# Kernel tuning notes

Hardware: AMD Instinct MI355X
Metric: run time of the kernel (lower is better)

## Reference

```python
import jax, jax.numpy as jnp
import numpy as np

N = 16384       # num nodes
E = 65536       # num edges (before self loops)
IN_DIM = 1536
HID = 1024
HEADS = 8
HD = HID // HEADS  # 128
NEG_SLOPE = 0.2
EPS = 1e-5


def _xavier(key, shape):
    fan_in, fan_out = shape[0], shape[-1]
    s = jnp.sqrt(6.0 / (fan_in + fan_out)).astype(jnp.float32)
    return jax.random.uniform(key, shape, jnp.float32, -s, s)


def setup_inputs() -> dict:
    key = jax.random.key(0)
    ks = jax.random.split(key, 32)
    inp = {
        "x": jax.random.normal(ks[0], (N, IN_DIM), jnp.float32),
        "edge_index": jax.random.randint(ks[1], (2, E), 0, N, dtype=jnp.int32),
        # input projection + norm1
        "W_in": _xavier(ks[2], (IN_DIM, HID)), "b_in": jnp.zeros((HID,), jnp.float32),
        "ln1_g": jnp.ones((HID,), jnp.float32), "ln1_b": jnp.zeros((HID,), jnp.float32),
        # GATv2 layer 1
        "g1_Wl": _xavier(ks[3], (HID, HID)), "g1_bl": jnp.zeros((HID,), jnp.float32),
        "g1_Wr": _xavier(ks[4], (HID, HID)), "g1_br": jnp.zeros((HID,), jnp.float32),
        "g1_att": _xavier(ks[5], (HEADS, HD)), "g1_bo": jnp.zeros((HID,), jnp.float32),
        "ln2_g": jnp.ones((HID,), jnp.float32), "ln2_b": jnp.zeros((HID,), jnp.float32),
        # GATv2 layer 2
        "g2_Wl": _xavier(ks[6], (HID, HID)), "g2_bl": jnp.zeros((HID,), jnp.float32),
        "g2_Wr": _xavier(ks[7], (HID, HID)), "g2_br": jnp.zeros((HID,), jnp.float32),
        "g2_att": _xavier(ks[8], (HEADS, HD)), "g2_bo": jnp.zeros((HID,), jnp.float32),
        "ln3_g": jnp.ones((HID,), jnp.float32), "ln3_b": jnp.zeros((HID,), jnp.float32),
        # scorer MLP 1024 -> 512 -> 128 -> 1
        "Ws1": _xavier(ks[9], (HID, 512)), "bs1": jnp.zeros((512,), jnp.float32),
        "Ws2": _xavier(ks[10], (512, 128)), "bs2": jnp.zeros((128,), jnp.float32),
        "Ws3": _xavier(ks[11], (128, 1)), "bs3": jnp.zeros((1,), jnp.float32),
    }
    return inp


def layer_norm(x, g, b):
    mu = jnp.mean(x, axis=-1, keepdims=True)
    var = jnp.var(x, axis=-1, keepdims=True)
    return (x - mu) * jax.lax.rsqrt(var + EPS) * g + b


def gatv2(h, src, dst, Wl, bl, Wr, br, att, bo):
    # GATv2Conv: x_j = lin_l(h)[src], x_i = lin_r(h)[dst]
    xl = (h @ Wl + bl).reshape(N, HEADS, HD)
    xr = (h @ Wr + br).reshape(N, HEADS, HD)
    e = jax.nn.leaky_relu(xl[src] + xr[dst], NEG_SLOPE)      # [E', H, C]
    logit = jnp.einsum('ehc,hc->eh', e, att)                  # [E', H]
    m = jax.ops.segment_max(logit, dst, num_segments=N)       # segment softmax over dst
    a = jnp.exp(logit - m[dst])
    denom = jax.ops.segment_sum(a, dst, num_segments=N)
    alpha = a / denom[dst]
    out = jax.ops.segment_sum(alpha[:, :, None] * xl[src], dst, num_segments=N)
    return out.reshape(N, HID) + bo


def reference(x, edge_index, W_in, b_in, ln1_g, ln1_b,
              g1_Wl, g1_bl, g1_Wr, g1_br, g1_att, g1_bo, ln2_g, ln2_b,
              g2_Wl, g2_bl, g2_Wr, g2_br, g2_att, g2_bo, ln3_g, ln3_b,
              Ws1, bs1, Ws2, bs2, Ws3, bs3):
    # PyG GATv2Conv adds self-loops by default
    loop = jnp.arange(N, dtype=edge_index.dtype)
    src = jnp.concatenate([edge_index[0], loop])
    dst = jnp.concatenate([edge_index[1], loop])

    h = jax.nn.gelu(layer_norm(x @ W_in + b_in, ln1_g, ln1_b), approximate=False)
    h1 = gatv2(h, src, dst, g1_Wl, g1_bl, g1_Wr, g1_br, g1_att, g1_bo)
    h = h + jax.nn.gelu(layer_norm(h1, ln2_g, ln2_b), approximate=False)
    h2 = gatv2(h, src, dst, g2_Wl, g2_bl, g2_Wr, g2_br, g2_att, g2_bo)
    h = h + jax.nn.gelu(layer_norm(h2, ln3_g, ln3_b), approximate=False)

    s = jax.nn.silu(h @ Ws1 + bs1)
    s = jax.nn.silu(s @ Ws2 + bs2)
    scores = (s @ Ws3 + bs3).squeeze(-1)   # [N]
    return scores, h
```

## Files before the change

kernel.cpp:

```cpp
#include <hip/hip_runtime.h>
#include <hip/hip_bf16.h>
#include <math.h>

#define N_NODES 16384
#define E_EDGES 65536
#define ET (E_EDGES + N_NODES)
#define IN_DIM 1536
#define HID 1024
#define XSTR 2048

typedef __attribute__((ext_vector_type(8))) short bf16x8;
typedef __attribute__((ext_vector_type(4))) float f32x4;

__device__ __forceinline__ unsigned short f2b(float f) {
  unsigned int u = __float_as_uint(f);
  u = (u + 0x7FFFu + ((u >> 16) & 1u)) >> 16;
  return (unsigned short)u;
}

__device__ __forceinline__ float b2f(unsigned short u) {
  return __uint_as_float((unsigned int)u << 16);
}

__device__ __forceinline__ void gload_lds16(const void* g, void* l) {
  __builtin_amdgcn_global_load_lds((const __attribute__((address_space(1))) void*)g,
                                   (__attribute__((address_space(3))) void*)l, 16, 0, 0);
}

__device__ __forceinline__ float gelu_exact(float y) {
  return 0.5f * y * (1.0f + erff(y * 0.70710678118654752f));
}

__global__ void conv_bf16_kernel(const float* __restrict__ in, unsigned short* __restrict__ out, int n4) {
  int i = blockIdx.x * 256 + threadIdx.x;
  if (i < n4) {
    float4 v = ((const float4*)in)[i];
    ushort4 o;
    o.x = f2b(v.x); o.y = f2b(v.y); o.z = f2b(v.z); o.w = f2b(v.w);
    ((ushort4*)out)[i] = o;
  }
}

__global__ void transpose_all_kernel(const float* __restrict__ W_in,
                                     const float* __restrict__ g1Wl, const float* __restrict__ g1Wr,
                                     const float* __restrict__ g2Wl, const float* __restrict__ g2Wr,
                                     const float* __restrict__ Ws1, const float* __restrict__ Ws2,
                                     unsigned short* __restrict__ WinT, unsigned short* __restrict__ g1WT,
                                     unsigned short* __restrict__ g2WT, unsigned short* __restrict__ Ws1T,
                                     unsigned short* __restrict__ Ws2T) {
  int bid = blockIdx.x;
  const float* src; unsigned short* dst; int K, N, tile;
  if (bid < 1536)      { src = W_in; dst = WinT;                          K = 1536; N = 1024; tile = bid; }
  else if (bid < 2560) { src = g1Wl; dst = g1WT;                         K = 1024; N = 1024; tile = bid - 1536; }
  else if (bid < 3584) { src = g1Wr; dst = g1WT + (size_t)1024 * 1024;   K = 1024; N = 1024; tile = bid - 2560; }
  else if (bid < 4608) { src = g2Wl; dst = g2WT;                         K = 1024; N = 1024; tile = bid - 3584; }
  else if (bid < 5632) { src = g2Wr; dst = g2WT + (size_t)1024 * 1024;   K = 1024; N = 1024; tile = bid - 4608; }
  else if (bid < 6144) { src = Ws1; dst = Ws1T;                          K = 1024; N = 512;  tile = bid - 5632; }
  else                 { src = Ws2; dst = Ws2T;                          K = 512;  N = 128;  tile = bid - 6144; }
  int nxt = N >> 5;
  int bx = (tile % nxt) * 32;
  int by = (tile / nxt) * 32;
  __shared__ float tilebuf[32][33];
  int tx = threadIdx.x, ty = threadIdx.y;
  #pragma unroll
  for (int i = 0; i < 32; i += 8)
    tilebuf[ty + i][tx] = src[(size_t)(by + ty + i) * N + bx + tx];
  __syncthreads();
  #pragma unroll
  for (int i = 0; i < 32; i += 8)
    dst[(size_t)(bx + ty + i) * K + by + tx] = f2b(tilebuf[tx][ty + i]);
}

template <int ACT, int WB>
__global__ __launch_bounds__(512)
void gemm_bf16_kernel(const unsigned short* __restrict__ A, const unsigned short* __restrict__ Bt,
                      const float* __restrict__ bias, const float* __restrict__ bias2, int nsplit,
                      float* __restrict__ C, unsigned short* __restrict__ Cb,
                      int M, int N, int K, int nx) {
  __shared__ unsigned short As[256 * 64];
  __shared__ unsigned short Bs[128 * 64];
  const int t = threadIdx.x;
  const int l = t & 63;
  const int w = t >> 6;
  const int wr = w >> 1, wc = w & 1;

  const int nwg = gridDim.x;
  const int bid = blockIdx.x;
  int tile = bid;
  if ((nwg & 7) == 0) {
    const int cpx = nwg >> 3;
    tile = (bid & 7) * cpx + (bid >> 3);
  }
  const int bm = (tile / nx) * 256;
  const int bn = (tile % nx) * 128;

  f32x4 acc[4][4];
  #pragma unroll
  for (int m = 0; m < 4; m++)
    #pragma unroll
    for (int n = 0; n < 4; n++) acc[m][n] = (f32x4){0.f, 0.f, 0.f, 0.f};

  const int srow = t >> 3;
  const int scolbsw = ((t & 7) * 16) ^ ((srow & 7) << 4);
  const unsigned short* Ag = A + (size_t)(bm + srow) * K + (scolbsw >> 1);
  const unsigned short* Bg = Bt + (size_t)(bn + srow) * K + (scolbsw >> 1);

  const int ar = wr * 64 + (l & 15);
  const int br = wc * 64 + (l & 15);
  const int kk2 = (l >> 4) * 16;
  const int swA = (ar & 7) << 4;
  const int swB = (br & 7) << 4;
  const char* Asb = (const char*)As;
  const char* Bsb = (const char*)Bs;

  for (int k0 = 0; k0 < K; k0 += 64) {
    #pragma unroll
    for (int i = 0; i < 4; i++)
      gload_lds16(Ag + (size_t)i * 64 * K + k0, (char*)As + t * 16 + i * 8192);
    #pragma unroll
    for (int i = 0; i < 2; i++)
      gload_lds16(Bg + (size_t)i * 64 * K + k0, (char*)Bs + t * 16 + i * 8192);
    __syncthreads();
    bf16x8 af[4], bfr[4];
    #pragma unroll
    for (int kh = 0; kh < 2; kh++) {
      const int kb = kk2 + kh * 64;
      #pragma unroll
      for (int m = 0; m < 4; m++)
        af[m] = *(const bf16x8*)(Asb + (ar + m * 16) * 128 + (kb ^ swA));
      #pragma unroll
      for (int n = 0; n < 4; n++)
        bfr[n] = *(const bf16x8*)(Bsb + (br + n * 16) * 128 + (kb ^ swB));
      #pragma unroll
      for (int m = 0; m < 4; m++)
        #pragma unroll
        for (int n = 0; n < 4; n++)
          acc[m][n] = __builtin_amdgcn_mfma_f32_16x16x32_bf16(af[m], bfr[n], acc[m][n], 0, 0, 0);
    }
    __syncthreads();
  }

  const int crow0 = bm + wr * 64 + (l >> 4) * 4;
  const int ccol0 = bn + wc * 64 + (l & 15);
  #pragma unroll
  for (int m = 0; m < 4; m++) {
    #pragma unroll
    for (int n = 0; n < 4; n++) {
      int col = ccol0 + n * 16;
      float bv = (col < nsplit) ? bias[col] : bias2[col - nsplit];
      #pragma unroll
      for (int v = 0; v < 4; v++) {
        int row = crow0 + m * 16 + v;
        float x = acc[m][n][v] + bv;
        if (ACT == 1) x = x / (1.0f + expf(-x));
        if (WB != 2) C[(size_t)row * N + col] = x;
        if (WB != 0) Cb[(size_t)row * N + col] = f2b(x);
      }
    }
  }
}

__global__ __launch_bounds__(256)
void ln_gelu_kernel(const unsigned short* __restrict__ cb, const float* __restrict__ g,
                    const float* __restrict__ b, unsigned short* __restrict__ hb) {
  int row = blockIdx.x;
  int t = threadIdx.x;
  int c0 = t * 4;
  ushort4 u = *(const ushort4*)(cb + (size_t)row * HID + c0);
  float v0 = b2f(u.x), v1 = b2f(u.y), v2 = b2f(u.z), v3 = b2f(u.w);
  float s = v0 + v1 + v2 + v3;
  float q = v0 * v0 + v1 * v1 + v2 * v2 + v3 * v3;
  #pragma unroll
  for (int off = 32; off; off >>= 1) {
    s += __shfl_xor(s, off);
    q += __shfl_xor(q, off);
  }
  __shared__ float rs[4], rq[4];
  int wv = t >> 6, l = t & 63;
  if (l == 0) { rs[wv] = s; rq[wv] = q; }
  __syncthreads();
  s = rs[0] + rs[1] + rs[2] + rs[3];
  q = rq[0] + rq[1] + rq[2] + rq[3];
  float mu = s * (1.0f / HID);
  float var = q * (1.0f / HID) - mu * mu;
  float rstd = rsqrtf(var + 1e-5f);
  const float4 gv = *(const float4*)(g + c0);
  const float4 bv = *(const float4*)(b + c0);
  ushort4 ob;
  ob.x = f2b(gelu_exact((v0 - mu) * rstd * gv.x + bv.x));
  ob.y = f2b(gelu_exact((v1 - mu) * rstd * gv.y + bv.y));
  ob.z = f2b(gelu_exact((v2 - mu) * rstd * gv.z + bv.z));
  ob.w = f2b(gelu_exact((v3 - mu) * rstd * gv.w + bv.w));
  *(ushort4*)(hb + (size_t)row * HID + c0) = ob;
}

__global__ void build_edges_kernel(const int* __restrict__ ei, int* __restrict__ srcA,
                                   int* __restrict__ dstA, int* __restrict__ deg) {
  int i = blockIdx.x * 256 + threadIdx.x;
  if (i >= ET) return;
  int s, d;
  if (i < E_EDGES) { s = ei[i]; d = ei[E_EDGES + i]; }
  else             { s = i - E_EDGES; d = s; }
  srcA[i] = s;
  dstA[i] = d;
  atomicAdd(&deg[d], 1);
}

__global__ __launch_bounds__(1024)
void scan16k_kernel(const int* __restrict__ deg, int* __restrict__ rowstart) {
  __shared__ int s[1024];
  int t = threadIdx.x;
  int local[16];
  int sum = 0;
  #pragma unroll
  for (int i = 0; i < 16; i++) { local[i] = deg[t * 16 + i]; sum += local[i]; }
  s[t] = sum;
  __syncthreads();
  for (int off = 1; off < 1024; off <<= 1) {
    int v = (t >= off) ? s[t - off] : 0;
    __syncthreads();
    s[t] += v;
    __syncthreads();
  }
  int run = s[t] - sum;
  #pragma unroll
  for (int i = 0; i < 16; i++) { rowstart[t * 16 + i] = run; run += local[i]; }
  if (t == 1023) rowstart[16384] = run;
}

__global__ void scatter_edges_kernel(const int* __restrict__ srcA, const int* __restrict__ dstA,
                                     const int* __restrict__ rowstart, int* __restrict__ cursor,
                                     int* __restrict__ src_csr) {
  int i = blockIdx.x * 256 + threadIdx.x;
  if (i >= ET) return;
  int d = dstA[i];
  int pos = atomicAdd(&cursor[d], 1);
  src_csr[rowstart[d] + pos] = srcA[i];
}

template <int WRITE_H>
__global__ __launch_bounds__(256)
void gat_fused_kernel(const unsigned short* __restrict__ xe, const float* __restrict__ att,
                      const int* __restrict__ src_csr, const int* __restrict__ rowstart,
                      const float* __restrict__ bo, const float* __restrict__ lng,
                      const float* __restrict__ lnb, float* __restrict__ h,
                      unsigned short* __restrict__ hb) {
  const int l = threadIdx.x & 63;
  const int nid = blockIdx.x * 4 + (threadIdx.x >> 6);
  const int beg = rowstart[nid], end = rowstart[nid + 1];
  const int cb = l * 16;

  float xrf[16], attf[16];
  {
    const unsigned short* xrd = xe + (size_t)nid * XSTR + 1024 + cb;
    bf16x8 r0 = *(const bf16x8*)xrd;
    bf16x8 r1 = *(const bf16x8*)(xrd + 8);
    #pragma unroll
    for (int j = 0; j < 8; j++) {
      xrf[j] = b2f((unsigned short)r0[j]);
      xrf[j + 8] = b2f((unsigned short)r1[j]);
    }
    #pragma unroll
    for (int j = 0; j < 4; j++) {
      float4 a = *(const float4*)(att + cb + j * 4);
      attf[j * 4] = a.x; attf[j * 4 + 1] = a.y;
      attf[j * 4 + 2] = a.z; attf[j * 4 + 3] = a.w;
    }
  }

  float m = -1e30f, den = 0.f;
  float acc[16];
  #pragma unroll
  for (int j = 0; j < 16; j++) acc[j] = 0.f;

  bf16x8 xa0, xa1, xb0, xb1;
  if (beg < end) {
    const unsigned short* p = xe + (size_t)src_csr[beg] * XSTR + cb;
    xa0 = *(const bf16x8*)p;
    xa1 = *(const bf16x8*)(p + 8);
  }
  if (beg + 1 < end) {
    const unsigned short* p = xe + (size_t)src_csr[beg + 1] * XSTR + cb;
    xb0 = *(const bf16x8*)p;
    xb1 = *(const bf16x8*)(p + 8);
  }
  for (int e = beg; e < end; ++e) {
    bf16x8 c0 = xa0, c1 = xa1;
    xa0 = xb0; xa1 = xb1;
    if (e + 2 < end) {
      const unsigned short* p = xe + (size_t)src_csr[e + 2] * XSTR + cb;
      xb0 = *(const bf16x8*)p;
      xb1 = *(const bf16x8*)(p + 8);
    }
    float xf[16];
    #pragma unroll
    for (int j = 0; j < 8; j++) {
      xf[j] = b2f((unsigned short)c0[j]);
      xf[j + 8] = b2f((unsigned short)c1[j]);
    }
    float lg = 0.f;
    #pragma unroll
    for (int j = 0; j < 16; j++) {
      float u = xf[j] + xrf[j];
      u = fmaxf(u, 0.2f * u);
      lg = fmaf(u, attf[j], lg);
    }
    lg += __shfl_xor(lg, 1);
    lg += __shfl_xor(lg, 2);
    lg += __shfl_xor(lg, 4);
    if (__all(lg <= m + 8.f)) {
      float wgt = expf(lg - m);
      den += wgt;
      #pragma unroll
      for (int j = 0; j < 16; j++) acc[j] = fmaf(wgt, xf[j], acc[j]);
    } else {
      float nm = fmaxf(m, lg);
      float sc = expf(m - nm);
      float wgt = expf(lg - nm);
      den = den * sc + wgt;
      #pragma unroll
      for (int j = 0; j < 16; j++) acc[j] = fmaf(wgt, xf[j], acc[j] * sc);
      m = nm;
    }
  }

  float inv = 1.0f / den;
  float v[16];
  #pragma unroll
  for (int j = 0; j < 4; j++) {
    float4 b = *(const float4*)(bo + cb + j * 4);
    v[j * 4] = acc[j * 4] * inv + b.x;
    v[j * 4 + 1] = acc[j * 4 + 1] * inv + b.y;
    v[j * 4 + 2] = acc[j * 4 + 2] * inv + b.z;
    v[j * 4 + 3] = acc[j * 4 + 3] * inv + b.w;
  }
  float s = 0.f, q = 0.f;
  #pragma unroll
  for (int j = 0; j < 16; j++) { s += v[j]; q += v[j] * v[j]; }
  #pragma unroll
  for (int off = 32; off; off >>= 1) {
    s += __shfl_xor(s, off);
    q += __shfl_xor(q, off);
  }
  float mu = s * (1.0f / HID);
  float var = q * (1.0f / HID) - mu * mu;
  float rstd = rsqrtf(var + 1e-5f);

  float* hr = h + (size_t)nid * HID + cb;
  unsigned short* hbr = hb + (size_t)nid * HID + cb;
  #pragma unroll
  for (int j = 0; j < 4; j++) {
    float4 gv = *(const float4*)(lng + cb + j * 4);
    float4 bb = *(const float4*)(lnb + cb + j * 4);
    ushort4 hu = *(const ushort4*)(hbr + j * 4);
    float o0 = b2f(hu.x) + gelu_exact((v[j * 4] - mu) * rstd * gv.x + bb.x);
    float o1 = b2f(hu.y) + gelu_exact((v[j * 4 + 1] - mu) * rstd * gv.y + bb.y);
    float o2 = b2f(hu.z) + gelu_exact((v[j * 4 + 2] - mu) * rstd * gv.z + bb.z);
    float o3 = b2f(hu.w) + gelu_exact((v[j * 4 + 3] - mu) * rstd * gv.w + bb.w);
    if (WRITE_H) *(float4*)(hr + j * 4) = (float4){o0, o1, o2, o3};
    ushort4 ob;
    ob.x = f2b(o0); ob.y = f2b(o1); ob.z = f2b(o2); ob.w = f2b(o3);
    *(ushort4*)(hbr + j * 4) = ob;
  }
}

__global__ __launch_bounds__(256)
void score_kernel(const float* __restrict__ s2, const float* __restrict__ Ws3,
                  const float* __restrict__ bs3, float* __restrict__ out) {
  int nid = blockIdx.x * 4 + (threadIdx.x >> 6);
  int l = threadIdx.x & 63;
  const float* r = s2 + (size_t)nid * 128;
  float a = r[l] * Ws3[l] + r[l + 64] * Ws3[l + 64];
  #pragma unroll
  for (int off = 32; off; off >>= 1) a += __shfl_xor(a, off);
  if (l == 0) out[nid] = a + bs3[0];
}

extern "C" void kernel_launch(void* const* d_in, const int* in_sizes, int n_in,
                              void* d_out, int out_size, void* d_ws, size_t ws_size,
                              hipStream_t stream) {
  const float* x    = (const float*)d_in[0];
  const int*   ei   = (const int*)  d_in[1];
  const float* W_in = (const float*)d_in[2];
  const float* b_in = (const float*)d_in[3];
  const float* ln1g = (const float*)d_in[4];
  const float* ln1b = (const float*)d_in[5];
  const float* g1Wl = (const float*)d_in[6];
  const float* g1bl = (const float*)d_in[7];
  const float* g1Wr = (const float*)d_in[8];
  const float* g1br = (const float*)d_in[9];
  const float* g1att= (const float*)d_in[10];
  const float* g1bo = (const float*)d_in[11];
  const float* ln2g = (const float*)d_in[12];
  const float* ln2b = (const float*)d_in[13];
  const float* g2Wl = (const float*)d_in[14];
  const float* g2bl = (const float*)d_in[15];
  const float* g2Wr = (const float*)d_in[16];
  const float* g2br = (const float*)d_in[17];
  const float* g2att= (const float*)d_in[18];
  const float* g2bo = (const float*)d_in[19];
  const float* ln3g = (const float*)d_in[20];
  const float* ln3b = (const float*)d_in[21];
  const float* Ws1  = (const float*)d_in[22];
  const float* bs1  = (const float*)d_in[23];
  const float* Ws2  = (const float*)d_in[24];
  const float* bs2  = (const float*)d_in[25];
  const float* Ws3  = (const float*)d_in[26];
  const float* bs3  = (const float*)d_in[27];

  float* scores = (float*)d_out;
  float* h      = (float*)d_out + N_NODES;

  char* wsp = (char*)d_ws;
  size_t off = 0;
  auto alloc = [&](size_t bytes) -> char* {
    char* p = wsp + off;
    off += (bytes + 255) & ~(size_t)255;
    return p;
  };
  unsigned short* xb    = (unsigned short*)alloc((size_t)N_NODES * IN_DIM * 2);
  unsigned short* WinT  = (unsigned short*)alloc((size_t)HID * IN_DIM * 2);
  unsigned short* g1WT  = (unsigned short*)alloc((size_t)XSTR * HID * 2);
  unsigned short* g2WT  = (unsigned short*)alloc((size_t)XSTR * HID * 2);
  unsigned short* Ws1T  = (unsigned short*)alloc((size_t)512 * HID * 2);
  unsigned short* Ws2T  = (unsigned short*)alloc((size_t)128 * 512 * 2);
  unsigned short* hb    = (unsigned short*)alloc((size_t)N_NODES * HID * 2);
  unsigned short* s1b   = (unsigned short*)alloc((size_t)N_NODES * 512 * 2);
  unsigned short* xe    = (unsigned short*)alloc((size_t)N_NODES * XSTR * 2);
  float* C      = (float*)alloc((size_t)N_NODES * HID * 4);
  int* srcA     = (int*)alloc((size_t)ET * 4);
  int* dstA     = (int*)alloc((size_t)ET * 4);
  int* deg      = (int*)alloc(65536);
  int* cursor   = (int*)alloc(65536);
  int* rowstart = (int*)alloc(65544);
  int* src_csr  = (int*)alloc((size_t)ET * 4);
  unsigned short* cbp = (unsigned short*)C;

  conv_bf16_kernel<<<(N_NODES * IN_DIM / 4 + 255) / 256, 256, 0, stream>>>(x, xb, N_NODES * IN_DIM / 4);
  transpose_all_kernel<<<6208, dim3(32, 8), 0, stream>>>(W_in, g1Wl, g1Wr, g2Wl, g2Wr, Ws1, Ws2,
                                                         WinT, g1WT, g2WT, Ws1T, Ws2T);

  hipMemsetAsync(deg, 0, 131072, stream);
  build_edges_kernel<<<ET / 256, 256, 0, stream>>>(ei, srcA, dstA, deg);
  scan16k_kernel<<<1, 1024, 0, stream>>>(deg, rowstart);
  scatter_edges_kernel<<<ET / 256, 256, 0, stream>>>(srcA, dstA, rowstart, cursor, src_csr);

  gemm_bf16_kernel<0, 2><<<(N_NODES / 256) * (HID / 128), 512, 0, stream>>>(
      xb, WinT, b_in, b_in, HID, nullptr, cbp, N_NODES, HID, IN_DIM, HID / 128);
  ln_gelu_kernel<<<N_NODES, 256, 0, stream>>>(cbp, ln1g, ln1b, hb);

  gemm_bf16_kernel<0, 2><<<(N_NODES / 256) * (XSTR / 128), 512, 0, stream>>>(
      hb, g1WT, g1bl, g1br, HID, nullptr, xe, N_NODES, XSTR, HID, XSTR / 128);
  gat_fused_kernel<0><<<N_NODES / 4, 256, 0, stream>>>(xe, g1att, src_csr, rowstart, g1bo,
                                                       ln2g, ln2b, h, hb);

  gemm_bf16_kernel<0, 2><<<(N_NODES / 256) * (XSTR / 128), 512, 0, stream>>>(
      hb, g2WT, g2bl, g2br, HID, nullptr, xe, N_NODES, XSTR, HID, XSTR / 128);
  gat_fused_kernel<1><<<N_NODES / 4, 256, 0, stream>>>(xe, g2att, src_csr, rowstart, g2bo,
                                                       ln3g, ln3b, h, hb);

  gemm_bf16_kernel<1, 2><<<(N_NODES / 256) * (512 / 128), 512, 0, stream>>>(
      hb, Ws1T, bs1, bs1, 512, nullptr, s1b, N_NODES, 512, HID, 512 / 128);
  gemm_bf16_kernel<1, 0><<<(N_NODES / 256) * 1, 512, 0, stream>>>(
      s1b, Ws2T, bs2, bs2, 128, C, nullptr, N_NODES, 128, 512, 1);
  score_kernel<<<N_NODES / 4, 256, 0, stream>>>(C, Ws3, bs3, scores);
}
```

Baseline: 440.3 us.

## Fuse fp32-to-bf16 input conversion into first GEMM; grid-stride GAT kernel

```diff
diff --git a/kernel.cpp b/kernel.cpp
--- a/kernel.cpp
+++ b/kernel.cpp
@@ -29,16 +29,6 @@
 
 __device__ __forceinline__ float gelu_exact(float y) {
   return 0.5f * y * (1.0f + erff(y * 0.70710678118654752f));
-}
-
-__global__ void conv_bf16_kernel(const float* __restrict__ in, unsigned short* __restrict__ out, int n4) {
-  int i = blockIdx.x * 256 + threadIdx.x;
-  if (i < n4) {
-    float4 v = ((const float4*)in)[i];
-    ushort4 o;
-    o.x = f2b(v.x); o.y = f2b(v.y); o.z = f2b(v.z); o.w = f2b(v.w);
-    ((ushort4*)out)[i] = o;
-  }
 }
 
 __global__ void transpose_all_kernel(const float* __restrict__ W_in,
@@ -71,9 +61,9 @@
     dst[(size_t)(bx + ty + i) * K + by + tx] = f2b(tilebuf[tx][ty + i]);
 }
 
-template <int ACT, int WB>
+template <int ACT, int WB, int FP32A>
 __global__ __launch_bounds__(512)
-void gemm_bf16_kernel(const unsigned short* __restrict__ A, const unsigned short* __restrict__ Bt,
+void gemm_bf16_kernel(const void* __restrict__ Av, const unsigned short* __restrict__ Bt,
                       const float* __restrict__ bias, const float* __restrict__ bias2, int nsplit,
                       float* __restrict__ C, unsigned short* __restrict__ Cb,
                       int M, int N, int K, int nx) {
@@ -102,7 +92,8 @@
 
   const int srow = t >> 3;
   const int scolbsw = ((t & 7) * 16) ^ ((srow & 7) << 4);
-  const unsigned short* Ag = A + (size_t)(bm + srow) * K + (scolbsw >> 1);
+  const unsigned short* Ag = (const unsigned short*)Av + (size_t)(bm + srow) * K + (scolbsw >> 1);
+  const float* Ag32 = (const float*)Av + (size_t)(bm + srow) * K + (scolbsw >> 1);
   const unsigned short* Bg = Bt + (size_t)(bn + srow) * K + (scolbsw >> 1);
 
   const int ar = wr * 64 + (l & 15);
@@ -114,9 +105,24 @@
   const char* Bsb = (const char*)Bs;
 
   for (int k0 = 0; k0 < K; k0 += 64) {
-    #pragma unroll
-    for (int i = 0; i < 4; i++)
-      gload_lds16(Ag + (size_t)i * 64 * K + k0, (char*)As + t * 16 + i * 8192);
+    if (FP32A) {
+      #pragma unroll
+      for (int i = 0; i < 4; i++) {
+        const float* s = Ag32 + (size_t)i * 64 * K + k0;
+        float4 f0 = *(const float4*)s;
+        float4 f1 = *(const float4*)(s + 4);
+        bf16x8 wv;
+        wv[0] = (short)f2b(f0.x); wv[1] = (short)f2b(f0.y);
+        wv[2] = (short)f2b(f0.z); wv[3] = (short)f2b(f0.w);
+        wv[4] = (short)f2b(f1.x); wv[5] = (short)f2b(f1.y);
+        wv[6] = (short)f2b(f1.z); wv[7] = (short)f2b(f1.w);
+        *(bf16x8*)((char*)As + t * 16 + i * 8192) = wv;
+      }
+    } else {
+      #pragma unroll
+      for (int i = 0; i < 4; i++)
+        gload_lds16(Ag + (size_t)i * 64 * K + k0, (char*)As + t * 16 + i * 8192);
+    }
     #pragma unroll
     for (int i = 0; i < 2; i++)
       gload_lds16(Bg + (size_t)i * 64 * K + k0, (char*)Bs + t * 16 + i * 8192);
@@ -246,121 +252,126 @@
                       const float* __restrict__ lnb, float* __restrict__ h,
                       unsigned short* __restrict__ hb) {
   const int l = threadIdx.x & 63;
-  const int nid = blockIdx.x * 4 + (threadIdx.x >> 6);
-  const int beg = rowstart[nid], end = rowstart[nid + 1];
   const int cb = l * 16;
-
-  float xrf[16], attf[16];
-  {
-    const unsigned short* xrd = xe + (size_t)nid * XSTR + 1024 + cb;
-    bf16x8 r0 = *(const bf16x8*)xrd;
-    bf16x8 r1 = *(const bf16x8*)(xrd + 8);
-    #pragma unroll
-    for (int j = 0; j < 8; j++) {
-      xrf[j] = b2f((unsigned short)r0[j]);
-      xrf[j + 8] = b2f((unsigned short)r1[j]);
-    }
-    #pragma unroll
-    for (int j = 0; j < 4; j++) {
-      float4 a = *(const float4*)(att + cb + j * 4);
-      attf[j * 4] = a.x; attf[j * 4 + 1] = a.y;
-      attf[j * 4 + 2] = a.z; attf[j * 4 + 3] = a.w;
-    }
-  }
-
-  float m = -1e30f, den = 0.f;
-  float acc[16];
-  #pragma unroll
-  for (int j = 0; j < 16; j++) acc[j] = 0.f;
-
-  bf16x8 xa0, xa1, xb0, xb1;
-  if (beg < end) {
-    const unsigned short* p = xe + (size_t)src_csr[beg] * XSTR + cb;
-    xa0 = *(const bf16x8*)p;
-    xa1 = *(const bf16x8*)(p + 8);
-  }
-  if (beg + 1 < end) {
-    const unsigned short* p = xe + (size_t)src_csr[beg + 1] * XSTR + cb;
-    xb0 = *(const bf16x8*)p;
-    xb1 = *(const bf16x8*)(p + 8);
-  }
-  for (int e = beg; e < end; ++e) {
-    bf16x8 c0 = xa0, c1 = xa1;
-    xa0 = xb0; xa1 = xb1;
-    if (e + 2 < end) {
-      const unsigned short* p = xe + (size_t)src_csr[e + 2] * XSTR + cb;
+  const int stride = gridDim.x * 4;
+
+  float attf[16];
+  #pragma unroll
+  for (int j = 0; j < 4; j++) {
+    float4 a = *(const float4*)(att + cb + j * 4);
+    attf[j * 4] = a.x; attf[j * 4 + 1] = a.y;
+    attf[j * 4 + 2] = a.z; attf[j * 4 + 3] = a.w;
+  }
+
+  for (int nid = blockIdx.x * 4 + (threadIdx.x >> 6); nid < N_NODES; nid += stride) {
+    const int beg = rowstart[nid], end = rowstart[nid + 1];
+
+    float xrf[16];
+    {
+      const unsigned short* xrd = xe + (size_t)nid * XSTR + 1024 + cb;
+      bf16x8 r0 = *(const bf16x8*)xrd;
+      bf16x8 r1 = *(const bf16x8*)(xrd + 8);
+      #pragma unroll
+      for (int j = 0; j < 8; j++) {
+        xrf[j] = b2f((unsigned short)r0[j]);
+        xrf[j + 8] = b2f((unsigned short)r1[j]);
+      }
+    }
+
+    float m = -1e30f, den = 0.f;
+    float acc[16];
+    #pragma unroll
+    for (int j = 0; j < 16; j++) acc[j] = 0.f;
+
+    bf16x8 xa0, xa1, xb0, xb1;
+    if (beg < end) {
+      const unsigned short* p = xe + (size_t)src_csr[beg] * XSTR + cb;
+      xa0 = *(const bf16x8*)p;
+      xa1 = *(const bf16x8*)(p + 8);
+    }
+    if (beg + 1 < end) {
+      const unsigned short* p = xe + (size_t)src_csr[beg + 1] * XSTR + cb;
       xb0 = *(const bf16x8*)p;
       xb1 = *(const bf16x8*)(p + 8);
     }
-    float xf[16];
-    #pragma unroll
-    for (int j = 0; j < 8; j++) {
-      xf[j] = b2f((unsigned short)c0[j]);
-      xf[j + 8] = b2f((unsigned short)c1[j]);
-    }
-    float lg = 0.f;
-    #pragma unroll
-    for (int j = 0; j < 16; j++) {
-      float u = xf[j] + xrf[j];
-      u = fmaxf(u, 0.2f * u);
-      lg = fmaf(u, attf[j], lg);
-    }
-    lg += __shfl_xor(lg, 1);
-    lg += __shfl_xor(lg, 2);
-    lg += __shfl_xor(lg, 4);
-    if (__all(lg <= m + 8.f)) {
-      float wgt = expf(lg - m);
-      den += wgt;
-      #pragma unroll
-      for (int j = 0; j < 16; j++) acc[j] = fmaf(wgt, xf[j], acc[j]);
-    } else {
-      float nm = fmaxf(m, lg);
-      float sc = expf(m - nm);
-      float wgt = expf(lg - nm);
-      den = den * sc + wgt;
-      #pragma unroll
-      for (int j = 0; j < 16; j++) acc[j] = fmaf(wgt, xf[j], acc[j] * sc);
-      m = nm;
-    }
-  }
-
-  float inv = 1.0f / den;
-  float v[16];
-  #pragma unroll
-  for (int j = 0; j < 4; j++) {
-    float4 b = *(const float4*)(bo + cb + j * 4);
-    v[j * 4] = acc[j * 4] * inv + b.x;
-    v[j * 4 + 1] = acc[j * 4 + 1] * inv + b.y;
-    v[j * 4 + 2] = acc[j * 4 + 2] * inv + b.z;
-    v[j * 4 + 3] = acc[j * 4 + 3] * inv + b.w;
-  }
-  float s = 0.f, q = 0.f;
-  #pragma unroll
-  for (int j = 0; j < 16; j++) { s += v[j]; q += v[j] * v[j]; }
-  #pragma unroll
-  for (int off = 32; off; off >>= 1) {
-    s += __shfl_xor(s, off);
-    q += __shfl_xor(q, off);
-  }
-  float mu = s * (1.0f / HID);
-  float var = q * (1.0f / HID) - mu * mu;
-  float rstd = rsqrtf(var + 1e-5f);
-
-  float* hr = h + (size_t)nid * HID + cb;
-  unsigned short* hbr = hb + (size_t)nid * HID + cb;
-  #pragma unroll
-  for (int j = 0; j < 4; j++) {
-    float4 gv = *(const float4*)(lng + cb + j * 4);
-    float4 bb = *(const float4*)(lnb + cb + j * 4);
-    ushort4 hu = *(const ushort4*)(hbr + j * 4);
-    float o0 = b2f(hu.x) + gelu_exact((v[j * 4] - mu) * rstd * gv.x + bb.x);
-    float o1 = b2f(hu.y) + gelu_exact((v[j * 4 + 1] - mu) * rstd * gv.y + bb.y);
-    float o2 = b2f(hu.z) + gelu_exact((v[j * 4 + 2] - mu) * rstd * gv.z + bb.z);
-    float o3 = b2f(hu.w) + gelu_exact((v[j * 4 + 3] - mu) * rstd * gv.w + bb.w);
-    if (WRITE_H) *(float4*)(hr + j * 4) = (float4){o0, o1, o2, o3};
-    ushort4 ob;
-    ob.x = f2b(o0); ob.y = f2b(o1); ob.z = f2b(o2); ob.w = f2b(o3);
-    *(ushort4*)(hbr + j * 4) = ob;
+    for (int e = beg; e < end; ++e) {
+      bf16x8 c0 = xa0, c1 = xa1;
+      xa0 = xb0; xa1 = xb1;
+      if (e + 2 < end) {
+        const unsigned short* p = xe + (size_t)src_csr[e + 2] * XSTR + cb;
+        xb0 = *(const bf16x8*)p;
+        xb1 = *(const bf16x8*)(p + 8);
+      }
+      float xf[16];
+      #pragma unroll
+      for (int j = 0; j < 8; j++) {
+        xf[j] = b2f((unsigned short)c0[j]);
+        xf[j + 8] = b2f((unsigned short)c1[j]);
+      }
+      float lg = 0.f;
+      #pragma unroll
+      for (int j = 0; j < 16; j++) {
+        float u = xf[j] + xrf[j];
+        u = fmaxf(u, 0.2f * u);
+        lg = fmaf(u, attf[j], lg);
+      }
+      lg += __shfl_xor(lg, 1);
+      lg += __shfl_xor(lg, 2);
+      lg += __shfl_xor(lg, 4);
+      if (__all(lg <= m + 8.f)) {
+        float wgt = expf(lg - m);
+        den += wgt;
+        #pragma unroll
+        for (int j = 0; j < 16; j++) acc[j] = fmaf(wgt, xf[j], acc[j]);
+      } else {
+        float nm = fmaxf(m, lg);
+        float sc = expf(m - nm);
+        float wgt = expf(lg - nm);
+        den = den * sc + wgt;
+        #pragma unroll
+        for (int j = 0; j < 16; j++) acc[j] = fmaf(wgt, xf[j], acc[j] * sc);
+        m = nm;
+      }
+    }
+
+    float inv = 1.0f / den;
+    float v[16];
+    #pragma unroll
+    for (int j = 0; j < 4; j++) {
+      float4 b = *(const float4*)(bo + cb + j * 4);
+      v[j * 4] = acc[j * 4] * inv + b.x;
+      v[j * 4 + 1] = acc[j * 4 + 1] * inv + b.y;
+      v[j * 4 + 2] = acc[j * 4 + 2] * inv + b.z;
+      v[j * 4 + 3] = acc[j * 4 + 3] * inv + b.w;
+    }
+    float s = 0.f, q = 0.f;
+    #pragma unroll
+    for (int j = 0; j < 16; j++) { s += v[j]; q += v[j] * v[j]; }
+    #pragma unroll
+    for (int off = 32; off; off >>= 1) {
+      s += __shfl_xor(s, off);
+      q += __shfl_xor(q, off);
+    }
+    float mu = s * (1.0f / HID);
+    float var = q * (1.0f / HID) - mu * mu;
+    float rstd = rsqrtf(var + 1e-5f);
+
+    float* hr = h + (size_t)nid * HID + cb;
+    unsigned short* hbr = hb + (size_t)nid * HID + cb;
+    #pragma unroll
+    for (int j = 0; j < 4; j++) {
+      float4 gv = *(const float4*)(lng + cb + j * 4);
+      float4 bb = *(const float4*)(lnb + cb + j * 4);
+      ushort4 hu = *(const ushort4*)(hbr + j * 4);
+      float o0 = b2f(hu.x) + gelu_exact((v[j * 4] - mu) * rstd * gv.x + bb.x);
+      float o1 = b2f(hu.y) + gelu_exact((v[j * 4 + 1] - mu) * rstd * gv.y + bb.y);
+      float o2 = b2f(hu.z) + gelu_exact((v[j * 4 + 2] - mu) * rstd * gv.z + bb.z);
+      float o3 = b2f(hu.w) + gelu_exact((v[j * 4 + 3] - mu) * rstd * gv.w + bb.w);
+      if (WRITE_H) *(float4*)(hr + j * 4) = (float4){o0, o1, o2, o3};
+      ushort4 ob;
+      ob.x = f2b(o0); ob.y = f2b(o1); ob.z = f2b(o2); ob.w = f2b(o3);
+      *(ushort4*)(hbr + j * 4) = ob;
+    }
   }
 }
 
@@ -418,7 +429,6 @@
     off += (bytes + 255) & ~(size_t)255;
     return p;
   };
-  unsigned short* xb    = (unsigned short*)alloc((size_t)N_NODES * IN_DIM * 2);
   unsigned short* WinT  = (unsigned short*)alloc((size_t)HID * IN_DIM * 2);
   unsigned short* g1WT  = (unsigned short*)alloc((size_t)XSTR * HID * 2);
   unsigned short* g2WT  = (unsigned short*)alloc((size_t)XSTR * HID * 2);
@@ -436,7 +446,6 @@
   int* src_csr  = (int*)alloc((size_t)ET * 4);
   unsigned short* cbp = (unsigned short*)C;
 
-  conv_bf16_kernel<<<(N_NODES * IN_DIM / 4 + 255) / 256, 256, 0, stream>>>(x, xb, N_NODES * IN_DIM / 4);
   transpose_all_kernel<<<6208, dim3(32, 8), 0, stream>>>(W_in, g1Wl, g1Wr, g2Wl, g2Wr, Ws1, Ws2,
                                                          WinT, g1WT, g2WT, Ws1T, Ws2T);
 
@@ -445,23 +454,23 @@
   scan16k_kernel<<<1, 1024, 0, stream>>>(deg, rowstart);
   scatter_edges_kernel<<<ET / 256, 256, 0, stream>>>(srcA, dstA, rowstart, cursor, src_csr);
 
-  gemm_bf16_kernel<0, 2><<<(N_NODES / 256) * (HID / 128), 512, 0, stream>>>(
-      xb, WinT, b_in, b_in, HID, nullptr, cbp, N_NODES, HID, IN_DIM, HID / 128);
+  gemm_bf16_kernel<0, 2, 1><<<(N_NODES / 256) * (HID / 128), 512, 0, stream>>>(
+      x, WinT, b_in, b_in, HID, nullptr, cbp, N_NODES, HID, IN_DIM, HID / 128);
   ln_gelu_kernel<<<N_NODES, 256, 0, stream>>>(cbp, ln1g, ln1b, hb);
 
-  gemm_bf16_kernel<0, 2><<<(N_NODES / 256) * (XSTR / 128), 512, 0, stream>>>(
+  gemm_bf16_kernel<0, 2, 0><<<(N_NODES / 256) * (XSTR / 128), 512, 0, stream>>>(
       hb, g1WT, g1bl, g1br, HID, nullptr, xe, N_NODES, XSTR, HID, XSTR / 128);
-  gat_fused_kernel<0><<<N_NODES / 4, 256, 0, stream>>>(xe, g1att, src_csr, rowstart, g1bo,
-                                                       ln2g, ln2b, h, hb);
-
-  gemm_bf16_kernel<0, 2><<<(N_NODES / 256) * (XSTR / 128), 512, 0, stream>>>(
+  gat_fused_kernel<0><<<2048, 256, 0, stream>>>(xe, g1att, src_csr, rowstart, g1bo,
+                                                ln2g, ln2b, h, hb);
+
+  gemm_bf16_kernel<0, 2, 0><<<(N_NODES / 256) * (XSTR / 128), 512, 0, stream>>>(
       hb, g2WT, g2bl, g2br, HID, nullptr, xe, N_NODES, XSTR, HID, XSTR / 128);
-  gat_fused_kernel<1><<<N_NODES / 4, 256, 0, stream>>>(xe, g2att, src_csr, rowstart, g2bo,
-                                                       ln3g, ln3b, h, hb);
-
-  gemm_bf16_kernel<1, 2><<<(N_NODES / 256) * (512 / 128), 512, 0, stream>>>(
+  gat_fused_kernel<1><<<2048, 256, 0, stream>>>(xe, g2att, src_csr, rowstart, g2bo,
+                                                ln3g, ln3b, h, hb);
+
+  gemm_bf16_kernel<1, 2, 0><<<(N_NODES / 256) * (512 / 128), 512, 0, stream>>>(
       hb, Ws1T, bs1, bs1, 512, nullptr, s1b, N_NODES, 512, HID, 512 / 128);
-  gemm_bf16_kernel<1, 0><<<(N_NODES / 256) * 1, 512, 0, stream>>>(
+  gemm_bf16_kernel<1, 0, 0><<<(N_NODES / 256) * 1, 512, 0, stream>>>(
       s1b, Ws2T, bs2, bs2, 128, C, nullptr, N_NODES, 128, 512, 1);
   score_kernel<<<N_NODES / 4, 256, 0, stream>>>(C, Ws3, bs3, scores);
 }
```

New measurement: 482.0 us. +9.5%, slower.

## Add 256x256-tile 8-wave GEMM with phased LDS double-buffered pipeline

Applied to the files above, without the earlier changes.

```diff
diff --git a/kernel.cpp b/kernel.cpp
--- a/kernel.cpp
+++ b/kernel.cpp
@@ -69,6 +69,137 @@
   #pragma unroll
   for (int i = 0; i < 32; i += 8)
     dst[(size_t)(bx + ty + i) * K + by + tx] = f2b(tilebuf[tx][ty + i]);
+}
+
+#define VM4() asm volatile("s_waitcnt vmcnt(4)" ::: "memory")
+#define VM0() asm volatile("s_waitcnt vmcnt(0)" ::: "memory")
+
+#define STGA(kh, Tn)                                                           \
+  do {                                                                         \
+    const unsigned short* s_ = Ag + (size_t)(Tn) * 64 + (kh) * 32;             \
+    gload_lds16(s_, Anxt + (kh) * 16384 + t * 16);                             \
+    gload_lds16(s_ + rowK128, Anxt + (kh) * 16384 + 8192 + t * 16);            \
+  } while (0)
+#define STGB(kh, Tn)                                                           \
+  do {                                                                         \
+    const unsigned short* s_ = Bg + (size_t)(Tn) * 64 + (kh) * 32;             \
+    gload_lds16(s_, Bnxt + (kh) * 16384 + t * 16);                             \
+    gload_lds16(s_ + rowK128, Bnxt + (kh) * 16384 + 8192 + t * 16);            \
+  } while (0)
+
+#define PHASE(kh, mh, STG_STMT, VM_STMT)                                       \
+  {                                                                            \
+    const char* Ap_ = Acur + (kh) * 16384;                                     \
+    const char* Bp_ = Bcur + (kh) * 16384;                                     \
+    bf16x8 af_[4], bf_[4];                                                     \
+    _Pragma("unroll") for (int m_ = 0; m_ < 4; m_++)                           \
+      af_[m_] = *(const bf16x8*)(Ap_ + (ar + ((mh) * 4 + m_) * 16) * 64 + (kk2 ^ swA)); \
+    _Pragma("unroll") for (int n_ = 0; n_ < 4; n_++)                           \
+      bf_[n_] = *(const bf16x8*)(Bp_ + (br + n_ * 16) * 64 + (kk2 ^ swB));     \
+    STG_STMT;                                                                  \
+    VM_STMT;                                                                   \
+    asm volatile("" ::: "memory");                                             \
+    __builtin_amdgcn_s_barrier();                                              \
+    asm volatile("s_waitcnt lgkmcnt(0)" ::: "memory");                         \
+    __builtin_amdgcn_sched_barrier(0);                                         \
+    __builtin_amdgcn_s_setprio(1);                                             \
+    _Pragma("unroll") for (int m_ = 0; m_ < 4; m_++)                           \
+      _Pragma("unroll") for (int n_ = 0; n_ < 4; n_++)                         \
+        acc[(mh) * 4 + m_][n_] = __builtin_amdgcn_mfma_f32_16x16x32_bf16(      \
+            af_[m_], bf_[n_], acc[(mh) * 4 + m_][n_], 0, 0, 0);                \
+    __builtin_amdgcn_s_setprio(0);                                             \
+    asm volatile("" ::: "memory");                                             \
+    __builtin_amdgcn_s_barrier();                                              \
+  }
+
+template <int WB>
+__global__ __launch_bounds__(512, 1)
+void gemm8p_kernel(const unsigned short* __restrict__ A, const unsigned short* __restrict__ Bt,
+                   const float* __restrict__ bias, const float* __restrict__ bias2, int nsplit,
+                   float* __restrict__ C, unsigned short* __restrict__ Cb,
+                   int M, int N, int K, int nx) {
+  __shared__ char Abuf[2][32768];
+  __shared__ char Bbuf[2][32768];
+  const int t = threadIdx.x;
+  const int l = t & 63;
+  const int w = t >> 6;
+  const int wr = w >> 2, wc = w & 3;
+
+  const int nwg = gridDim.x;
+  const int cpx = nwg >> 3;
+  const int bid = blockIdx.x;
+  const int tl = (bid & 7) * cpx + (bid >> 3);
+  const int bm = (tl / nx) * 256;
+  const int bn = (tl % nx) * 256;
+
+  f32x4 acc[8][4];
+  #pragma unroll
+  for (int m = 0; m < 8; m++)
+    #pragma unroll
+    for (int n = 0; n < 4; n++) acc[m][n] = (f32x4){0.f, 0.f, 0.f, 0.f};
+
+  const int srow = t >> 2;
+  const int scolb = ((t & 3) * 16) ^ (((srow >> 1) & 3) << 4);
+  const unsigned short* Ag = A + (size_t)(bm + srow) * K + (scolb >> 1);
+  const unsigned short* Bg = Bt + (size_t)(bn + srow) * K + (scolb >> 1);
+  const size_t rowK128 = (size_t)128 * K;
+
+  const int ar = wr * 128 + (l & 15);
+  const int br = wc * 64 + (l & 15);
+  const int kk2 = (l >> 4) * 16;
+  const int swA = ((ar >> 1) & 3) << 4;
+  const int swB = ((br >> 1) & 3) << 4;
+
+  const int NT = K >> 6;
+
+  gload_lds16(Ag, Abuf[0] + t * 16);
+  gload_lds16(Ag + rowK128, Abuf[0] + 8192 + t * 16);
+  gload_lds16(Bg, Bbuf[0] + t * 16);
+  gload_lds16(Bg + rowK128, Bbuf[0] + 8192 + t * 16);
+  gload_lds16(Ag + 32, Abuf[0] + 16384 + t * 16);
+  gload_lds16(Ag + 32 + rowK128, Abuf[0] + 16384 + 8192 + t * 16);
+  gload_lds16(Bg + 32, Bbuf[0] + 16384 + t * 16);
+  gload_lds16(Bg + 32 + rowK128, Bbuf[0] + 16384 + 8192 + t * 16);
+  VM4();
+  asm volatile("" ::: "memory");
+  __builtin_amdgcn_s_barrier();
+
+  for (int T = 0; T < NT - 1; ++T) {
+    const char* Acur = Abuf[T & 1];
+    const char* Bcur = Bbuf[T & 1];
+    char* Anxt = Abuf[(T + 1) & 1];
+    char* Bnxt = Bbuf[(T + 1) & 1];
+    PHASE(0, 0, STGA(0, T + 1), (void)0)
+    PHASE(0, 1, STGB(0, T + 1), VM4())
+    PHASE(1, 0, STGA(1, T + 1), (void)0)
+    PHASE(1, 1, STGB(1, T + 1), VM4())
+  }
+  {
+    const char* Acur = Abuf[(NT - 1) & 1];
+    const char* Bcur = Bbuf[(NT - 1) & 1];
+    PHASE(0, 0, (void)0, (void)0)
+    PHASE(0, 1, (void)0, VM0())
+    PHASE(1, 0, (void)0, (void)0)
+    PHASE(1, 1, (void)0, (void)0)
+  }
+
+  const int crow0 = bm + wr * 128 + (l >> 4) * 4;
+  const int ccol0 = bn + wc * 64 + (l & 15);
+  #pragma unroll
+  for (int m = 0; m < 8; m++) {
+    #pragma unroll
+    for (int n = 0; n < 4; n++) {
+      int col = ccol0 + n * 16;
+      float bv = (col < nsplit) ? bias[col] : bias2[col - nsplit];
+      #pragma unroll
+      for (int v = 0; v < 4; v++) {
+        int row = crow0 + m * 16 + v;
+        float x = acc[m][n][v] + bv;
+        if (WB != 2) C[(size_t)row * N + col] = x;
+        if (WB != 0) Cb[(size_t)row * N + col] = f2b(x);
+      }
+    }
+  }
 }
 
 template <int ACT, int WB>
@@ -445,17 +576,17 @@
   scan16k_kernel<<<1, 1024, 0, stream>>>(deg, rowstart);
   scatter_edges_kernel<<<ET / 256, 256, 0, stream>>>(srcA, dstA, rowstart, cursor, src_csr);
 
-  gemm_bf16_kernel<0, 2><<<(N_NODES / 256) * (HID / 128), 512, 0, stream>>>(
-      xb, WinT, b_in, b_in, HID, nullptr, cbp, N_NODES, HID, IN_DIM, HID / 128);
+  gemm8p_kernel<2><<<(N_NODES / 256) * (HID / 256), 512, 0, stream>>>(
+      xb, WinT, b_in, b_in, HID, nullptr, cbp, N_NODES, HID, IN_DIM, HID / 256);
   ln_gelu_kernel<<<N_NODES, 256, 0, stream>>>(cbp, ln1g, ln1b, hb);
 
-  gemm_bf16_kernel<0, 2><<<(N_NODES / 256) * (XSTR / 128), 512, 0, stream>>>(
-      hb, g1WT, g1bl, g1br, HID, nullptr, xe, N_NODES, XSTR, HID, XSTR / 128);
+  gemm8p_kernel<2><<<(N_NODES / 256) * (XSTR / 256), 512, 0, stream>>>(
+      hb, g1WT, g1bl, g1br, HID, nullptr, xe, N_NODES, XSTR, HID, XSTR / 256);
   gat_fused_kernel<0><<<N_NODES / 4, 256, 0, stream>>>(xe, g1att, src_csr, rowstart, g1bo,
                                                        ln2g, ln2b, h, hb);
 
-  gemm_bf16_kernel<0, 2><<<(N_NODES / 256) * (XSTR / 128), 512, 0, stream>>>(
-      hb, g2WT, g2bl, g2br, HID, nullptr, xe, N_NODES, XSTR, HID, XSTR / 128);
+  gemm8p_kernel<2><<<(N_NODES / 256) * (XSTR / 256), 512, 0, stream>>>(
+      hb, g2WT, g2bl, g2br, HID, nullptr, xe, N_NODES, XSTR, HID, XSTR / 256);
   gat_fused_kernel<1><<<N_NODES / 4, 256, 0, stream>>>(xe, g2att, src_csr, rowstart, g2bo,
                                                        ln3g, ln3b, h, hb);
 
```

After: 487.9 us. +10.8%, slower.
